# Optimization experiments

Measured on AMD Instinct MI355X. Metric: run time of the kernel, lower is better.

The kernel has to match this reference:

```python
import jax, jax.numpy as jnp
import numpy as np

B, S, D, H, K = 2, 1024, 1024, 16, 33  # batch, seq, d_model, heads, rel buckets (k+1)
d = D // H


def setup_inputs() -> dict:
    key = jax.random.key(0)
    ks = jax.random.split(key, 16)
    w = lambda k, shape: jax.random.normal(k, shape, dtype=jnp.float32) * 0.02
    return {
        "hidden_state": jax.random.normal(ks[0], (B, S, D), dtype=jnp.float32),
        "pos_indices": jax.random.randint(ks[1], (B, S, S), 0, K),
        "mask": jax.random.bernoulli(ks[2], 0.1, (B, 1, 1, S)),
        "Wq": w(ks[3], (D, D)), "bq": w(ks[4], (D,)),
        "Wk": w(ks[5], (D, D)), "bk": w(ks[6], (D,)),
        "Wv": w(ks[7], (D, D)), "bv": w(ks[8], (D,)),
        "Wo": w(ks[9], (D, D)), "bo": w(ks[10], (D,)),
        "rel_q": w(ks[11], (H, K, d)),
        "rel_k": w(ks[12], (H, K, d)),
        "rel_v": w(ks[13], (H, K, d)),
    }


def reference(hidden_state, pos_indices, mask, Wq, bq, Wk, bk, Wv, bv, Wo, bo,
              rel_q, rel_k, rel_v):
    b, s, dm = hidden_state.shape
    h, k_, dp = rel_q.shape
    # projections -> [B,H,S,d]
    def proj(x, W, bias):
        return (x @ W + bias).reshape(b, s, h, dp).transpose(0, 2, 1, 3)
    q = proj(hidden_state, Wq, bq)
    kk = proj(hidden_state, Wk, bk)
    v = proj(hidden_state, Wv, bv)
    # scale_factor = 1 (c2c) + 1 (rel_q) + 1 (rel_k)
    scale = 1.0 / np.sqrt(dp * 3).astype(np.float32)
    # content-to-content
    c2c = jnp.einsum("bhid,bhjd->bhij", q, kk) * scale
    idx = jnp.broadcast_to(pos_indices[:, None], (b, h, s, s))
    # position-to-content: raw [B,H,K,S], gathered along K with per-(i,j) bucket
    raw_p2c = jnp.einsum("hkd,bhjd->bhkj", rel_q, kk) * scale
    p2c = jnp.take_along_axis(raw_p2c, idx, axis=2)
    # content-to-position: raw [B,H,S,K], gathered along K
    raw_c2p = jnp.einsum("bhid,hkd->bhik", q, rel_k) * scale
    c2p = jnp.take_along_axis(raw_c2p, idx, axis=3)
    scores = c2c + p2c + c2p
    scores = jnp.where(mask, jnp.float32(-1e9), scores)
    probs = jax.nn.softmax(scores, axis=-1)  # dropout is identity in eval
    ctx = jnp.einsum("bhij,bhjd->bhid", probs, v)
    # value-side relative term: sum_j P[i,j] * rel_v[bucket(i,j)]
    oh = jax.nn.one_hot(pos_indices, k_, dtype=probs.dtype)  # [B,S,S,K]
    agg = jnp.einsum("bhij,bijk->bhik", probs, oh)
    ctx = ctx + jnp.einsum("bhik,hkd->bhid", agg, rel_v)
    out = ctx.transpose(0, 2, 1, 3).reshape(b, s, dm)
    return out @ Wo + bo
```

## Files before the change

kernel.cpp:

```cpp
#include <hip/hip_runtime.h>
#include <hip/hip_bf16.h>

#define B_ 2
#define S_ 1024
#define D_ 1024
#define H_ 16
#define K_ 33
#define DH 64
#define SCALE 0.07216878364870322f
#define LOG2E 1.4426950408889634f
#define SCALEL (SCALE * LOG2E)
#define FXS 32768.0f
#define FXI (1.0f / 32768.0f)

typedef __attribute__((ext_vector_type(8))) short bf16x8;
typedef __attribute__((ext_vector_type(4))) float f32x4;

__device__ __forceinline__ float b2f(unsigned short u) {
    return __uint_as_float(((unsigned int)u) << 16);
}
__device__ __forceinline__ unsigned short f2b(float f) {
    unsigned int u = __float_as_uint(f);
    u += 0x7FFFu + ((u >> 16) & 1u);
    return (unsigned short)(u >> 16);
}
__device__ __forceinline__ float ldf(const void* p, int i, int f32) {
    return f32 ? ((const float*)p)[i] : b2f(((const unsigned short*)p)[i]);
}
__device__ __forceinline__ float4 ldf4(const void* p, int i, int f32) {
    if (f32) return *(const float4*)((const float*)p + i);
    ushort4 u = *(const ushort4*)((const unsigned short*)p + i);
    return make_float4(b2f(u.x), b2f(u.y), b2f(u.z), b2f(u.w));
}
__device__ __forceinline__ float4 ldb4(const unsigned short* p, int i) {
    ushort4 u = *(const ushort4*)(p + i);
    return make_float4(b2f(u.x), b2f(u.y), b2f(u.z), b2f(u.w));
}

__global__ __launch_bounds__(256) void prep(const void* __restrict__ hidden,
                                            const void* __restrict__ mask,
                                            int* __restrict__ flags,
                                            float* __restrict__ mflag) {
    __shared__ int cnt;
    __shared__ int mev[6];
    const int t = threadIdx.x;
    if (t == 0) cnt = 0;
    if (t < 6) mev[t] = 0;
    __syncthreads();
    const unsigned short* hu = (const unsigned short*)hidden;
    int c = 0;
    for (int i = t; i < 2048; i += 256) {
        int e = (hu[i] >> 7) & 0xFF;
        if (e >= 0x8E) c++;
    }
    if (c) atomicAdd(&cnt, c);
    const unsigned char* mb = (const unsigned char*)mask;
    int e_bf = 0, e_f32 = 0, e_f64 = 0, e_f16 = 0, e_u8 = 0;
    for (int p = t; p < 2048; p += 256) {
        unsigned char v = mb[p];
        if ((p & 7) == 6 && v == 0xF0) e_f64 = 1;
        if ((p & 3) == 1 && v == 0x3F) e_bf = 1;
        if ((p & 3) == 3 && v == 0x3F) e_f32 = 1;
        if ((p & 1) == 1 && v == 0x3C) e_f16 = 1;
        if ((p & 3) != 0 && v != 0) e_u8 = 1;
    }
    if (e_f64) atomicOr(&mev[5], 1);
    if (e_bf)  atomicOr(&mev[3], 1);
    if (e_f32) atomicOr(&mev[2], 1);
    if (e_f16) atomicOr(&mev[4], 1);
    if (e_u8)  atomicOr(&mev[1], 1);
    __syncthreads();
    const int f32flag = (cnt >= 8) ? 1 : 0;
    const int mm = mev[5] ? 5 : (mev[3] ? 3 : (mev[2] ? 2 : (mev[4] ? 4 : (mev[1] ? 1 : 0))));
    if (t == 0) { flags[0] = f32flag; flags[2] = mm; }
    for (int j = t; j < B_ * S_; j += 256) {
        int m;
        if (mm == 5)      m = (((const double*)mask)[j] != 0.0);
        else if (mm == 3 || mm == 4) m = (((const unsigned short*)mask)[j] != 0);
        else if (mm == 2) m = (((const float*)mask)[j] != 0.f);
        else if (mm == 1) m = (mb[j] != 0);
        else              m = (((const int*)mask)[j] != 0);
        mflag[j] = m ? 1.f : 0.f;
    }
}

__global__ __launch_bounds__(256) void pos_pack(const int* __restrict__ pos,
                                                unsigned char* __restrict__ pos8) {
    int i = blockIdx.x * 256 + threadIdx.x;
    if (i >= (B_ * S_ * S_) / 4) return;
    int4 p = *(const int4*)&pos[i * 4];
    uchar4 o;
    o.x = (unsigned char)min(max(p.x, 0), K_ - 1);
    o.y = (unsigned char)min(max(p.y, 0), K_ - 1);
    o.z = (unsigned char)min(max(p.z, 0), K_ - 1);
    o.w = (unsigned char)min(max(p.w, 0), K_ - 1);
    *(uchar4*)&pos8[i * 4] = o;
}

__global__ __launch_bounds__(256) void w_pack(const void* __restrict__ W0,
                                              const void* __restrict__ W1,
                                              const void* __restrict__ W2,
                                              const void* __restrict__ W3,
                                              const int* __restrict__ flags,
                                              unsigned short* __restrict__ T0,
                                              unsigned short* __restrict__ T1,
                                              unsigned short* __restrict__ T2,
                                              unsigned short* __restrict__ T3) {
    __shared__ unsigned short tl[64][66];
    const int f32u = flags[0];
    const int z = blockIdx.z;
    const void* W = z == 0 ? W0 : (z == 1 ? W1 : (z == 2 ? W2 : W3));
    unsigned short* T = z == 0 ? T0 : (z == 1 ? T1 : (z == 2 ? T2 : T3));
    const int k0 = blockIdx.y * 64, n0 = blockIdx.x * 64;
    const int t = threadIdx.x;
    {
        int kr = t >> 2, nc = (t & 3) * 16;
#pragma unroll
        for (int u = 0; u < 4; ++u) {
            float4 v = ldf4(W, (k0 + kr) * 1024 + n0 + nc + u * 4, f32u);
            tl[kr][nc + u * 4 + 0] = f2b(v.x);
            tl[kr][nc + u * 4 + 1] = f2b(v.y);
            tl[kr][nc + u * 4 + 2] = f2b(v.z);
            tl[kr][nc + u * 4 + 3] = f2b(v.w);
        }
    }
    __syncthreads();
    {
        int nr = t >> 2, kc = (t & 3) * 16;
        unsigned short o[16];
#pragma unroll
        for (int u = 0; u < 16; ++u) o[u] = tl[kc + u][nr];
#pragma unroll
        for (int u = 0; u < 4; ++u)
            *(ushort4*)&T[(n0 + nr) * 1024 + k0 + kc + u * 4] = *(ushort4*)&o[u * 4];
    }
}

__global__ __launch_bounds__(256, 3) void gemm_qkv_mfma(const void* __restrict__ X,
                                                        const void* __restrict__ W0,
                                                        const void* __restrict__ W1,
                                                        const void* __restrict__ W2,
                                                        const unsigned short* __restrict__ T0,
                                                        const unsigned short* __restrict__ T1,
                                                        const unsigned short* __restrict__ T2,
                                                        const void* __restrict__ b0,
                                                        const void* __restrict__ b1,
                                                        const void* __restrict__ b2,
                                                        const int* __restrict__ flags, int useT,
                                                        unsigned short* __restrict__ q,
                                                        unsigned short* __restrict__ kk_,
                                                        unsigned short* __restrict__ v) {
    __shared__ unsigned short Asl[128][40];
    __shared__ unsigned short Bsl[64][40];
    const int f32u = flags[0];
    const int z = blockIdx.z;
    const void* W = z == 0 ? W0 : (z == 1 ? W1 : W2);
    const unsigned short* WT = z == 0 ? T0 : (z == 1 ? T1 : T2);
    const void* bias = z == 0 ? b0 : (z == 1 ? b1 : b2);
    unsigned short* outp = z == 0 ? q : (z == 1 ? kk_ : v);
    const int m0 = blockIdx.y * 128, n0 = blockIdx.x * 64;
    const int t = threadIdx.x;
    const int w = t >> 6, lane = t & 63;
    const int wr = w >> 1, wc = w & 1;
    const int lm = lane & 15, lg = lane >> 4;

    const int am = t >> 1, ac16 = (t & 1) * 16;
    const int bn = t >> 2, bk8 = (t & 3) * 8;
    const int fbn = t & 63, fbkq = (t >> 6) * 8;

    f32x4 acc[4][2] = {};
    float4 pa[4];
    ushort4 tb0, tb1;
    float pbx[8];

    {
        int base = (m0 + am) * 1024 + ac16;
#pragma unroll
        for (int u = 0; u < 4; ++u) pa[u] = ldf4(X, base + u * 4, f32u);
        if (useT) {
            const ushort4* s = (const ushort4*)&WT[(n0 + bn) * 1024 + bk8];
            tb0 = s[0]; tb1 = s[1];
        } else {
#pragma unroll
            for (int qi = 0; qi < 8; ++qi)
                pbx[qi] = ldf(W, (fbkq + qi) * 1024 + n0 + fbn, f32u);
        }
    }

    for (int k0 = 0; k0 < 1024; k0 += 32) {
        {
#pragma unroll
            for (int u = 0; u < 4; ++u) {
                ushort4 uv = {f2b(pa[u].x), f2b(pa[u].y), f2b(pa[u].z), f2b(pa[u].w)};
                *(ushort4*)&Asl[am][ac16 + u * 4] = uv;
            }
            if (useT) {
                *(ushort4*)&Bsl[bn][bk8] = tb0;
                *(ushort4*)&Bsl[bn][bk8 + 4] = tb1;
            } else {
#pragma unroll
                for (int qi = 0; qi < 8; qi += 2) {
                    unsigned int pk = (unsigned int)f2b(pbx[qi]) |
                                      ((unsigned int)f2b(pbx[qi + 1]) << 16);
                    *(unsigned int*)&Bsl[fbn][fbkq + qi] = pk;
                }
            }
        }
        __syncthreads();
        if (k0 + 32 < 1024) {
            int kn = k0 + 32;
            int base = (m0 + am) * 1024 + kn + ac16;
#pragma unroll
            for (int u = 0; u < 4; ++u) pa[u] = ldf4(X, base + u * 4, f32u);
            if (useT) {
                const ushort4* s = (const ushort4*)&WT[(n0 + bn) * 1024 + kn + bk8];
                tb0 = s[0]; tb1 = s[1];
            } else {
#pragma unroll
                for (int qi = 0; qi < 8; ++qi)
                    pbx[qi] = ldf(W, (kn + fbkq + qi) * 1024 + n0 + fbn, f32u);
            }
        }
        bf16x8 af[4], bfr[2];
#pragma unroll
        for (int mi = 0; mi < 4; ++mi)
            af[mi] = *(const bf16x8*)&Asl[wr * 64 + mi * 16 + lm][lg * 8];
#pragma unroll
        for (int nj = 0; nj < 2; ++nj)
            bfr[nj] = *(const bf16x8*)&Bsl[wc * 32 + nj * 16 + lm][lg * 8];
#pragma unroll
        for (int mi = 0; mi < 4; ++mi)
#pragma unroll
            for (int nj = 0; nj < 2; ++nj)
                acc[mi][nj] = __builtin_amdgcn_mfma_f32_16x16x32_bf16(af[mi], bfr[nj],
                                                                      acc[mi][nj], 0, 0, 0);
        __syncthreads();
    }
#pragma unroll
    for (int nj = 0; nj < 2; ++nj) {
        int n = n0 + wc * 32 + nj * 16 + lm;
        float bv = ldf(bias, n, f32u);
        int hh = n >> 6, dd = n & 63;
#pragma unroll
        for (int mi = 0; mi < 4; ++mi) {
#pragma unroll
            for (int r = 0; r < 4; ++r) {
                int m = m0 + wr * 64 + mi * 16 + lg * 4 + r;
                int bb = m >> 10, ii = m & 1023;
                outp[((bb * H_ + hh) * S_ + ii) * DH + dd] = f2b(acc[mi][nj][r] + bv);
            }
        }
    }
}

__global__ __launch_bounds__(256, 3) void gemm_out_mfma(const unsigned short* __restrict__ X,
                                                        const void* __restrict__ W,
                                                        const unsigned short* __restrict__ WT,
                                                        const void* __restrict__ bias,
                                                        const int* __restrict__ flags, int useT,
                                                        float* __restrict__ out) {
    __shared__ unsigned short Asl[128][40];
    __shared__ unsigned short Bsl[64][40];
    const int f32u = flags[0];
    const int m0 = blockIdx.y * 128, n0 = blockIdx.x * 64;
    const int t = threadIdx.x;
    const int w = t >> 6, lane = t & 63;
    const int wr = w >> 1, wc = w & 1;
    const int lm = lane & 15, lg = lane >> 4;

    const int am = t >> 1, ac16 = (t & 1) * 16;
    const int bn = t >> 2, bk8 = (t & 3) * 8;
    const int fbn = t & 63, fbkq = (t >> 6) * 8;

    f32x4 acc[4][2] = {};
    ushort4 pa[4];
    ushort4 tb0, tb1;
    float pbx[8];

    {
        const ushort4* src = (const ushort4*)&X[(m0 + am) * 1024 + ac16];
#pragma unroll
        for (int u = 0; u < 4; ++u) pa[u] = src[u];
        if (useT) {
            const ushort4* s = (const ushort4*)&WT[(n0 + bn) * 1024 + bk8];
            tb0 = s[0]; tb1 = s[1];
        } else {
#pragma unroll
            for (int qi = 0; qi < 8; ++qi)
                pbx[qi] = ldf(W, (fbkq + qi) * 1024 + n0 + fbn, f32u);
        }
    }

    for (int k0 = 0; k0 < 1024; k0 += 32) {
        {
#pragma unroll
            for (int u = 0; u < 4; ++u) *(ushort4*)&Asl[am][ac16 + u * 4] = pa[u];
            if (useT) {
                *(ushort4*)&Bsl[bn][bk8] = tb0;
                *(ushort4*)&Bsl[bn][bk8 + 4] = tb1;
            } else {
#pragma unroll
                for (int qi = 0; qi < 8; qi += 2) {
                    unsigned int pk = (unsigned int)f2b(pbx[qi]) |
                                      ((unsigned int)f2b(pbx[qi + 1]) << 16);
                    *(unsigned int*)&Bsl[fbn][fbkq + qi] = pk;
                }
            }
        }
        __syncthreads();
        if (k0 + 32 < 1024) {
            int kn = k0 + 32;
            const ushort4* src = (const ushort4*)&X[(m0 + am) * 1024 + kn + ac16];
#pragma unroll
            for (int u = 0; u < 4; ++u) pa[u] = src[u];
            if (useT) {
                const ushort4* s = (const ushort4*)&WT[(n0 + bn) * 1024 + kn + bk8];
                tb0 = s[0]; tb1 = s[1];
            } else {
#pragma unroll
                for (int qi = 0; qi < 8; ++qi)
                    pbx[qi] = ldf(W, (kn + fbkq + qi) * 1024 + n0 + fbn, f32u);
            }
        }
        bf16x8 af[4], bfr[2];
#pragma unroll
        for (int mi = 0; mi < 4; ++mi)
            af[mi] = *(const bf16x8*)&Asl[wr * 64 + mi * 16 + lm][lg * 8];
#pragma unroll
        for (int nj = 0; nj < 2; ++nj)
            bfr[nj] = *(const bf16x8*)&Bsl[wc * 32 + nj * 16 + lm][lg * 8];
#pragma unroll
        for (int mi = 0; mi < 4; ++mi)
#pragma unroll
            for (int nj = 0; nj < 2; ++nj)
                acc[mi][nj] = __builtin_amdgcn_mfma_f32_16x16x32_bf16(af[mi], bfr[nj],
                                                                      acc[mi][nj], 0, 0, 0);
        __syncthreads();
    }
#pragma unroll
    for (int nj = 0; nj < 2; ++nj) {
        int n = n0 + wc * 32 + nj * 16 + lm;
        float bv = ldf(bias, n, f32u);
#pragma unroll
        for (int mi = 0; mi < 4; ++mi) {
#pragma unroll
            for (int r = 0; r < 4; ++r) {
                int m = m0 + wr * 64 + mi * 16 + lg * 4 + r;
                out[m * 1024 + n] = acc[mi][nj][r] + bv;
            }
        }
    }
}

__global__ __launch_bounds__(256) void rel_fused(const unsigned short* __restrict__ kws,
                                                 const unsigned short* __restrict__ qws,
                                                 const void* __restrict__ relq,
                                                 const void* __restrict__ relk,
                                                 const int* __restrict__ flags,
                                                 unsigned short* __restrict__ p2c,
                                                 unsigned short* __restrict__ c2p) {
    __shared__ float xt[64][68];
    __shared__ float rr[33][68];
    const int f32u = flags[0];
    const int bh = blockIdx.y, h = bh & 15;
    const int x0 = blockIdx.x * 64;
    const int t = threadIdx.x;
    if (blockIdx.z == 0) {
#pragma unroll
        for (int qq = 0; qq < 4; ++qq) {
            int idx = t + 256 * qq;
            int j = idx >> 4, d4 = idx & 15;
            *(float4*)&xt[j][d4 * 4] = ldb4(kws, (bh * S_ + x0 + j) * DH + d4 * 4);
        }
        for (int idx = t; idx < 33 * 16; idx += 256) {
            int k = idx >> 4, d4 = idx & 15;
            *(float4*)&rr[k][d4 * 4] = ldf4(relq, (h * K_ + k) * DH + d4 * 4, f32u);
        }
        __syncthreads();
        for (int o = t; o < 33 * 64; o += 256) {
            int k = o >> 6, j = o & 63;
            float s = 0.f;
#pragma unroll
            for (int d4 = 0; d4 < 16; ++d4) {
                float4 a = *(const float4*)&rr[k][d4 * 4];
                float4 b = *(const float4*)&xt[j][d4 * 4];
                s += a.x * b.x + a.y * b.y + a.z * b.z + a.w * b.w;
            }
            p2c[(bh * K_ + k) * S_ + x0 + j] = f2b(s * SCALEL);
        }
    } else {
#pragma unroll
        for (int qq = 0; qq < 4; ++qq) {
            int idx = t + 256 * qq;
            int i = idx >> 4, d4 = idx & 15;
            *(float4*)&xt[i][d4 * 4] = ldb4(qws, (bh * S_ + x0 + i) * DH + d4 * 4);
        }
        for (int idx = t; idx < 33 * 16; idx += 256) {
            int k = idx >> 4, d4 = idx & 15;
            *(float4*)&rr[k][d4 * 4] = ldf4(relk, (h * K_ + k) * DH + d4 * 4, f32u);
        }
        __syncthreads();
        for (int o = t; o < 64 * 33; o += 256) {
            int i = o / 33, k = o % 33;
            float s = 0.f;
#pragma unroll
            for (int d4 = 0; d4 < 16; ++d4) {
                float4 a = *(const float4*)&xt[i][d4 * 4];
                float4 b = *(const float4*)&rr[k][d4 * 4];
                s += a.x * b.x + a.y * b.y + a.z * b.z + a.w * b.w;
            }
            c2p[(bh * S_ + x0 + i) * K_ + k] = f2b(s * SCALEL);
        }
    }
}

#define PS_OFF   0
#define VT_OFF   32768
#define P2CS_OFF 32768
#define C2P_OFF  50176
#define AG_OFF   54528
#define RV_OFF   71936
#define MF_OFF   76160
#define ATTN_LDS 77184

__device__ __forceinline__ int ps_addr(int il, int jc) {
    return PS_OFF + il * 512 +
           ((jc * 2) ^ ((((il >> 2) & 3) << 5) ^ ((il & 3) << 4)));
}

__global__ __launch_bounds__(512, 4) void attn_mfma(const unsigned short* __restrict__ qws,
                                                    const unsigned short* __restrict__ kws,
                                                    const unsigned short* __restrict__ vws,
                                                    const unsigned short* __restrict__ p2c,
                                                    const unsigned short* __restrict__ c2p,
                                                    const float* __restrict__ mflag,
                                                    const unsigned char* __restrict__ pos8,
                                                    const int* __restrict__ pos32,
                                                    int use8,
                                                    const void* __restrict__ relv,
                                                    const int* __restrict__ flags,
                                                    unsigned short* __restrict__ ctxo) {
    extern __shared__ char smem[];
    const int f32u = flags[0];
    const int lin = blockIdx.y * 16 + blockIdx.x;
    const int logi = (lin & 7) * 64 + (lin >> 3);
    const int bh = logi >> 4, b = bh >> 4, h = bh & 15;
    const int i0 = (logi & 15) * 64;
    const int t = threadIdx.x;
    const int w = t >> 6, lane = t & 63;
    const int lm = lane & 15, lg = lane >> 4;
    const int iband = (w & 3) * 16;
    const int jh = w >> 2;
    const int dbase = jh * 32;

    unsigned int* agU = (unsigned int*)(smem + AG_OFF);
    unsigned short* c2pS = (unsigned short*)(smem + C2P_OFF);
    unsigned short* rvS = (unsigned short*)(smem + RV_OFF);
    unsigned char* mfS = (unsigned char*)(smem + MF_OFF);

    for (int idx = t; idx < 64 * 33; idx += 512) {
        int il = idx / 33, k = idx % 33;
        c2pS[il * 34 + k] = c2p[(bh * S_ + i0 + il) * K_ + k];
    }
    for (int idx = t; idx < 33 * 64; idx += 512) {
        int k = idx >> 6, d = idx & 63;
        rvS[k * 64 + d] = f2b(ldf(relv, (h * K_ + k) * DH + d, f32u));
    }
    for (int idx = t; idx < 1024; idx += 512)
        mfS[idx] = (mflag[b * S_ + idx] != 0.f) ? 1 : 0;
    for (int idx = t; idx < 2 * 64 * 34; idx += 512) agU[idx] = 0u;

    bf16x8 aq0 = *(const bf16x8*)&qws[(bh * S_ + i0 + iband + lm) * DH + lg * 8];
    bf16x8 aq1 = *(const bf16x8*)&qws[(bh * S_ + i0 + iband + lm) * DH + 32 + lg * 8];
    f32x4 acc0 = {}, acc1 = {};

    const int p2cbase = bh * K_ * S_;
    const int rowbase = (b * S_ + i0 + iband + lg * 4) * S_;
    const int agbase = jh * 2176;
    __syncthreads();

    for (int c = 0; c < 4; ++c) {
        for (int idx = t; idx < 33 * 32; idx += 512) {
            int k = idx >> 5, v8 = idx & 31;
            uint4 src = *(const uint4*)&p2c[p2cbase + k * S_ + c * 256 + v8 * 8];
            unsigned int* dst = (unsigned int*)(smem + P2CS_OFF + k * 516 + v8 * 16);
            dst[0] = src.x; dst[1] = src.y; dst[2] = src.z; dst[3] = src.w;
        }
        __syncthreads();

        for (int jt = 0; jt < 8; ++jt) {
            const int jc = jh * 128 + jt * 16 + lm;
            const int jcol = c * 256 + jc;
            int pb4[4];
            if (use8) {
#pragma unroll
                for (int r = 0; r < 4; ++r)
                    pb4[r] = pos8[rowbase + r * S_ + jcol];
            } else {
#pragma unroll
                for (int r = 0; r < 4; ++r) {
                    int p = pos32[rowbase + r * S_ + jcol];
                    pb4[r] = min(max(p, 0), K_ - 1);
                }
            }
            bf16x8 kf0 = *(const bf16x8*)&kws[(bh * S_ + jcol) * DH + lg * 8];
            bf16x8 kf1 = *(const bf16x8*)&kws[(bh * S_ + jcol) * DH + 32 + lg * 8];
            f32x4 a = {};
            a = __builtin_amdgcn_mfma_f32_16x16x32_bf16(aq0, kf0, a, 0, 0, 0);
            a = __builtin_amdgcn_mfma_f32_16x16x32_bf16(aq1, kf1, a, 0, 0, 0);
            const int masked = mfS[jcol];
#pragma unroll
            for (int r = 0; r < 4; ++r) {
                int il = iband + lg * 4 + r;
                int pb = pb4[r];
                float gv = b2f(*(const unsigned short*)(smem + P2CS_OFF + pb * 516 + jc * 2));
                float s = a[r] * SCALEL + gv + b2f(c2pS[il * 34 + pb]);
                float ev = masked ? 0.f : exp2f(s);
                *(unsigned short*)(smem + ps_addr(il, jc)) = f2b(ev);
                atomicAdd(&agU[agbase + il * 34 + pb], (unsigned int)(ev * FXS));
            }
        }
        __syncthreads();

        for (int st = 0; st < 2; ++st) {
#pragma unroll
            for (int u = 0; u < 2; ++u) {
                int idx = t + u * 512;
                int jj = idx >> 3;
                int a8 = idx & 7;
                int d0 = a8 * 8;
                int j = c * 256 + st * 128 + jj;
                bf16x8 vv = *(const bf16x8*)&vws[(bh * S_ + j) * DH + d0];
#pragma unroll
                for (int e = 0; e < 8; ++e) {
                    int ee = (e + a8) & 7;
                    *(unsigned short*)(smem + VT_OFF + (d0 + ee) * 272 + jj * 2) =
                        ((short*)&vv)[ee];
                }
            }
            __syncthreads();
#pragma unroll
            for (int ks = 0; ks < 4; ++ks) {
                int jcb = st * 128 + ks * 32 + lg * 8;
                bf16x8 af = *(const bf16x8*)(smem + ps_addr(iband + lm, jcb));
                bf16x8 b0 = *(const bf16x8*)(smem + VT_OFF + (dbase + lm) * 272 +
                                             (ks * 32 + lg * 8) * 2);
                bf16x8 b1 = *(const bf16x8*)(smem + VT_OFF + (dbase + 16 + lm) * 272 +
                                             (ks * 32 + lg * 8) * 2);
                acc0 = __builtin_amdgcn_mfma_f32_16x16x32_bf16(af, b0, acc0, 0, 0, 0);
                acc1 = __builtin_amdgcn_mfma_f32_16x16x32_bf16(af, b1, acc1, 0, 0, 0);
            }
            __syncthreads();
        }
    }

#pragma unroll
    for (int r = 0; r < 4; ++r) {
        int il = iband + lg * 4 + r;
        float rs = 0.f;
        float o0 = acc0[r], o1 = acc1[r];
        for (int kb = 0; kb < K_; ++kb) {
            float a = (float)(agU[il * 34 + kb] + agU[2176 + il * 34 + kb]) * FXI;
            rs += a;
            o0 += a * b2f(rvS[kb * 64 + dbase + lm]);
            o1 += a * b2f(rvS[kb * 64 + dbase + 16 + lm]);
        }
        float inv = 1.0f / rs;
        ctxo[(b * S_ + i0 + il) * D_ + h * DH + dbase + lm] = f2b(o0 * inv);
        ctxo[(b * S_ + i0 + il) * D_ + h * DH + dbase + 16 + lm] = f2b(o1 * inv);
    }
}

extern "C" void kernel_launch(void* const* d_in, const int* in_sizes, int n_in,
                              void* d_out, int out_size, void* d_ws, size_t ws_size,
                              hipStream_t stream) {
    const void* hidden = d_in[0];
    const void* pos = d_in[1];
    const void* mask = d_in[2];
    const void* Wq = d_in[3];
    const void* bq = d_in[4];
    const void* Wk = d_in[5];
    const void* bk = d_in[6];
    const void* Wv = d_in[7];
    const void* bv = d_in[8];
    const void* Wo = d_in[9];
    const void* bo = d_in[10];
    const void* rq = d_in[11];
    const void* rk = d_in[12];
    const void* rv = d_in[13];

    unsigned char* wsb = (unsigned char*)d_ws;
    size_t o = 0;
    int* flags = (int*)(wsb + o);            o += 256;
    float* mfl = (float*)(wsb + o);          o += 2048 * 4;
    o = (o + 255) & ~(size_t)255;
    unsigned short* qb   = (unsigned short*)(wsb + o); o += 4194304;
    unsigned short* kb   = (unsigned short*)(wsb + o); o += 4194304;
    unsigned short* vb   = (unsigned short*)(wsb + o); o += 4194304;
    unsigned short* p2cb = (unsigned short*)(wsb + o); o += 2162688;
    unsigned short* c2pb = (unsigned short*)(wsb + o); o += 2162688;
    unsigned short* ctxb = (unsigned short*)(wsb + o); o += 4194304;
    unsigned char* pos8  = (unsigned char*)(wsb + o);  o += 2097152;
    const int use8 = (ws_size >= o) ? 1 : 0;
    unsigned short* wTq = (unsigned short*)(wsb + o);  o += 2097152;
    unsigned short* wTk = (unsigned short*)(wsb + o);  o += 2097152;
    unsigned short* wTv = (unsigned short*)(wsb + o);  o += 2097152;
    unsigned short* wTo = (unsigned short*)(wsb + o);  o += 2097152;
    const int useT = (ws_size >= o) ? 1 : 0;

    float* out = (float*)d_out;
    const int* posi = (const int*)pos;

    hipFuncSetAttribute(reinterpret_cast<const void*>(attn_mfma),
                        hipFuncAttributeMaxDynamicSharedMemorySize, ATTN_LDS);

    dim3 tb(256);
    prep<<<dim3(1), tb, 0, stream>>>(hidden, mask, flags, mfl);
    if (use8) pos_pack<<<dim3(2048), tb, 0, stream>>>(posi, pos8);
    if (useT) w_pack<<<dim3(16, 16, 4), tb, 0, stream>>>(Wq, Wk, Wv, Wo, flags,
                                                         wTq, wTk, wTv, wTo);
    gemm_qkv_mfma<<<dim3(16, 16, 3), tb, 0, stream>>>(hidden, Wq, Wk, Wv,
                                                      wTq, wTk, wTv,
                                                      bq, bk, bv, flags, useT,
                                                      qb, kb, vb);
    rel_fused<<<dim3(16, 32, 2), tb, 0, stream>>>(kb, qb, rq, rk, flags, p2cb, c2pb);
    attn_mfma<<<dim3(16, 32), dim3(512), ATTN_LDS, stream>>>(qb, kb, vb, p2cb, c2pb, mfl,
                                                             pos8, posi, use8, rv, flags,
                                                             ctxb);
    gemm_out_mfma<<<dim3(16, 16), tb, 0, stream>>>(ctxb, Wo, wTo, bo, flags, useT,
                                                   out);
}
```

Measured before the change: 159.3 us.

## Fuse setup kernels into one launch and drop duplicated aggregate buffer

Merges the prep, pos_pack and w_pack kernels into a single setup_fused launch with block ranges for each task. Each weight-pack block re-sniffs the input dtype locally instead of waiting on the flags written by prep. This removes two launch gaps and a serial dependency. In the attention kernel the two half-copies of the fixed-point aggregate buffer become one shared buffer, which shrinks LDS use but puts more atomic contention on a single array.

```diff
diff --git a/kernel.cpp b/kernel.cpp
--- a/kernel.cpp
+++ b/kernel.cpp
@@ -36,24 +36,126 @@
     ushort4 u = *(const ushort4*)(p + i);
     return make_float4(b2f(u.x), b2f(u.y), b2f(u.z), b2f(u.w));
 }
+__device__ __forceinline__ int sniff_f32(const void* hidden) {
+    __shared__ int cnt;
+    if (threadIdx.x == 0) cnt = 0;
+    __syncthreads();
+    const unsigned short* hu = (const unsigned short*)hidden;
+    int c = 0;
+    for (int i = threadIdx.x; i < 2048; i += 256) {
+        int e = (hu[i] >> 7) & 0xFF;
+        if (e >= 0x8E) c++;
+    }
+    if (c) atomicAdd(&cnt, c);
+    __syncthreads();
+    return (cnt >= 8) ? 1 : 0;
+}
+
+__global__ __launch_bounds__(256) void setup_fused(const void* __restrict__ hidden,
+                                                   const void* __restrict__ mask,
+                                                   const int* __restrict__ pos,
+                                                   const void* __restrict__ W0,
+                                                   const void* __restrict__ W1,
+                                                   const void* __restrict__ W2,
+                                                   const void* __restrict__ W3,
+                                                   int* __restrict__ flags,
+                                                   float* __restrict__ mflag,
+                                                   unsigned char* __restrict__ pos8,
+                                                   unsigned short* __restrict__ T0,
+                                                   unsigned short* __restrict__ T1,
+                                                   unsigned short* __restrict__ T2,
+                                                   unsigned short* __restrict__ T3) {
+    const int bid = blockIdx.x;
+    const int t = threadIdx.x;
+    if (bid < 2048) {
+        int i = bid * 256 + t;
+        if (i < (B_ * S_ * S_) / 4) {
+            int4 p = *(const int4*)&pos[i * 4];
+            uchar4 o;
+            o.x = (unsigned char)min(max(p.x, 0), K_ - 1);
+            o.y = (unsigned char)min(max(p.y, 0), K_ - 1);
+            o.z = (unsigned char)min(max(p.z, 0), K_ - 1);
+            o.w = (unsigned char)min(max(p.w, 0), K_ - 1);
+            *(uchar4*)&pos8[i * 4] = o;
+        }
+        return;
+    }
+    if (bid < 3072) {
+        const int f32u = sniff_f32(hidden);
+        __shared__ unsigned short tl[64][66];
+        int r = bid - 2048;
+        int z = r >> 8;
+        int wy = (r & 255) >> 4, wx = r & 15;
+        const void* W = z == 0 ? W0 : (z == 1 ? W1 : (z == 2 ? W2 : W3));
+        unsigned short* T = z == 0 ? T0 : (z == 1 ? T1 : (z == 2 ? T2 : T3));
+        const int k0 = wy * 64, n0 = wx * 64;
+        {
+            int kr = t >> 2, nc = (t & 3) * 16;
+#pragma unroll
+            for (int u = 0; u < 4; ++u) {
+                float4 v = ldf4(W, (k0 + kr) * 1024 + n0 + nc + u * 4, f32u);
+                tl[kr][nc + u * 4 + 0] = f2b(v.x);
+                tl[kr][nc + u * 4 + 1] = f2b(v.y);
+                tl[kr][nc + u * 4 + 2] = f2b(v.z);
+                tl[kr][nc + u * 4 + 3] = f2b(v.w);
+            }
+        }
+        __syncthreads();
+        {
+            int nr = t >> 2, kc = (t & 3) * 16;
+            unsigned short o[16];
+#pragma unroll
+            for (int u = 0; u < 16; ++u) o[u] = tl[kc + u][nr];
+#pragma unroll
+            for (int u = 0; u < 4; ++u)
+                *(ushort4*)&T[(n0 + nr) * 1024 + k0 + kc + u * 4] = *(ushort4*)&o[u * 4];
+        }
+        return;
+    }
+    {
+        __shared__ int mev[6];
+        const int f32u = sniff_f32(hidden);
+        if (t < 6) mev[t] = 0;
+        __syncthreads();
+        const unsigned char* mb = (const unsigned char*)mask;
+        int e_bf = 0, e_f32 = 0, e_f64 = 0, e_f16 = 0, e_u8 = 0;
+        for (int p = t; p < 2048; p += 256) {
+            unsigned char v = mb[p];
+            if ((p & 7) == 6 && v == 0xF0) e_f64 = 1;
+            if ((p & 3) == 1 && v == 0x3F) e_bf = 1;
+            if ((p & 3) == 3 && v == 0x3F) e_f32 = 1;
+            if ((p & 1) == 1 && v == 0x3C) e_f16 = 1;
+            if ((p & 3) != 0 && v != 0) e_u8 = 1;
+        }
+        if (e_f64) atomicOr(&mev[5], 1);
+        if (e_bf)  atomicOr(&mev[3], 1);
+        if (e_f32) atomicOr(&mev[2], 1);
+        if (e_f16) atomicOr(&mev[4], 1);
+        if (e_u8)  atomicOr(&mev[1], 1);
+        __syncthreads();
+        const int mm = mev[5] ? 5 : (mev[3] ? 3 : (mev[2] ? 2 : (mev[4] ? 4 : (mev[1] ? 1 : 0))));
+        if (t == 0) { flags[0] = f32u; flags[2] = mm; }
+        for (int j = t; j < B_ * S_; j += 256) {
+            int m;
+            if (mm == 5)      m = (((const double*)mask)[j] != 0.0);
+            else if (mm == 3 || mm == 4) m = (((const unsigned short*)mask)[j] != 0);
+            else if (mm == 2) m = (((const float*)mask)[j] != 0.f);
+            else if (mm == 1) m = (mb[j] != 0);
+            else              m = (((const int*)mask)[j] != 0);
+            mflag[j] = m ? 1.f : 0.f;
+        }
+    }
+}
 
 __global__ __launch_bounds__(256) void prep(const void* __restrict__ hidden,
                                             const void* __restrict__ mask,
                                             int* __restrict__ flags,
                                             float* __restrict__ mflag) {
-    __shared__ int cnt;
     __shared__ int mev[6];
     const int t = threadIdx.x;
-    if (t == 0) cnt = 0;
+    const int f32u = sniff_f32(hidden);
     if (t < 6) mev[t] = 0;
     __syncthreads();
-    const unsigned short* hu = (const unsigned short*)hidden;
-    int c = 0;
-    for (int i = t; i < 2048; i += 256) {
-        int e = (hu[i] >> 7) & 0xFF;
-        if (e >= 0x8E) c++;
-    }
-    if (c) atomicAdd(&cnt, c);
     const unsigned char* mb = (const unsigned char*)mask;
     int e_bf = 0, e_f32 = 0, e_f64 = 0, e_f16 = 0, e_u8 = 0;
     for (int p = t; p < 2048; p += 256) {
@@ -70,9 +172,8 @@
     if (e_f16) atomicOr(&mev[4], 1);
     if (e_u8)  atomicOr(&mev[1], 1);
     __syncthreads();
-    const int f32flag = (cnt >= 8) ? 1 : 0;
     const int mm = mev[5] ? 5 : (mev[3] ? 3 : (mev[2] ? 2 : (mev[4] ? 4 : (mev[1] ? 1 : 0))));
-    if (t == 0) { flags[0] = f32flag; flags[2] = mm; }
+    if (t == 0) { flags[0] = f32u; flags[2] = mm; }
     for (int j = t; j < B_ * S_; j += 256) {
         int m;
         if (mm == 5)      m = (((const double*)mask)[j] != 0.0);
@@ -95,45 +196,6 @@
     o.z = (unsigned char)min(max(p.z, 0), K_ - 1);
     o.w = (unsigned char)min(max(p.w, 0), K_ - 1);
     *(uchar4*)&pos8[i * 4] = o;
-}
-
-__global__ __launch_bounds__(256) void w_pack(const void* __restrict__ W0,
-                                              const void* __restrict__ W1,
-                                              const void* __restrict__ W2,
-                                              const void* __restrict__ W3,
-                                              const int* __restrict__ flags,
-                                              unsigned short* __restrict__ T0,
-                                              unsigned short* __restrict__ T1,
-                                              unsigned short* __restrict__ T2,
-                                              unsigned short* __restrict__ T3) {
-    __shared__ unsigned short tl[64][66];
-    const int f32u = flags[0];
-    const int z = blockIdx.z;
-    const void* W = z == 0 ? W0 : (z == 1 ? W1 : (z == 2 ? W2 : W3));
-    unsigned short* T = z == 0 ? T0 : (z == 1 ? T1 : (z == 2 ? T2 : T3));
-    const int k0 = blockIdx.y * 64, n0 = blockIdx.x * 64;
-    const int t = threadIdx.x;
-    {
-        int kr = t >> 2, nc = (t & 3) * 16;
-#pragma unroll
-        for (int u = 0; u < 4; ++u) {
-            float4 v = ldf4(W, (k0 + kr) * 1024 + n0 + nc + u * 4, f32u);
-            tl[kr][nc + u * 4 + 0] = f2b(v.x);
-            tl[kr][nc + u * 4 + 1] = f2b(v.y);
-            tl[kr][nc + u * 4 + 2] = f2b(v.z);
-            tl[kr][nc + u * 4 + 3] = f2b(v.w);
-        }
-    }
-    __syncthreads();
-    {
-        int nr = t >> 2, kc = (t & 3) * 16;
-        unsigned short o[16];
-#pragma unroll
-        for (int u = 0; u < 16; ++u) o[u] = tl[kc + u][nr];
-#pragma unroll
-        for (int u = 0; u < 4; ++u)
-            *(ushort4*)&T[(n0 + nr) * 1024 + k0 + kc + u * 4] = *(ushort4*)&o[u * 4];
-    }
 }
 
 __global__ __launch_bounds__(256, 3) void gemm_qkv_mfma(const void* __restrict__ X,
@@ -419,9 +481,9 @@
 #define P2CS_OFF 32768
 #define C2P_OFF  50176
 #define AG_OFF   54528
-#define RV_OFF   71936
-#define MF_OFF   76160
-#define ATTN_LDS 77184
+#define RV_OFF   63232
+#define MF_OFF   67456
+#define ATTN_LDS 68480
 
 __device__ __forceinline__ int ps_addr(int il, int jc) {
     return PS_OFF + il * 512 +
@@ -468,7 +530,7 @@
     }
     for (int idx = t; idx < 1024; idx += 512)
         mfS[idx] = (mflag[b * S_ + idx] != 0.f) ? 1 : 0;
-    for (int idx = t; idx < 2 * 64 * 34; idx += 512) agU[idx] = 0u;
+    for (int idx = t; idx < 64 * 34; idx += 512) agU[idx] = 0u;
 
     bf16x8 aq0 = *(const bf16x8*)&qws[(bh * S_ + i0 + iband + lm) * DH + lg * 8];
     bf16x8 aq1 = *(const bf16x8*)&qws[(bh * S_ + i0 + iband + lm) * DH + 32 + lg * 8];
@@ -476,7 +538,6 @@
 
     const int p2cbase = bh * K_ * S_;
     const int rowbase = (b * S_ + i0 + iband + lg * 4) * S_;
-    const int agbase = jh * 2176;
     __syncthreads();
 
     for (int c = 0; c < 4; ++c) {
@@ -517,7 +578,7 @@
                 float s = a[r] * SCALEL + gv + b2f(c2pS[il * 34 + pb]);
                 float ev = masked ? 0.f : exp2f(s);
                 *(unsigned short*)(smem + ps_addr(il, jc)) = f2b(ev);
-                atomicAdd(&agU[agbase + il * 34 + pb], (unsigned int)(ev * FXS));
+                atomicAdd(&agU[il * 34 + pb], (unsigned int)(ev * FXS));
             }
         }
         __syncthreads();
@@ -560,7 +621,7 @@
         float rs = 0.f;
         float o0 = acc0[r], o1 = acc1[r];
         for (int kb = 0; kb < K_; ++kb) {
-            float a = (float)(agU[il * 34 + kb] + agU[2176 + il * 34 + kb]) * FXI;
+            float a = (float)agU[il * 34 + kb] * FXI;
             rs += a;
             o0 += a * b2f(rvS[kb * 64 + dbase + lm]);
             o1 += a * b2f(rvS[kb * 64 + dbase + 16 + lm]);
@@ -615,10 +676,13 @@
                         hipFuncAttributeMaxDynamicSharedMemorySize, ATTN_LDS);
 
     dim3 tb(256);
-    prep<<<dim3(1), tb, 0, stream>>>(hidden, mask, flags, mfl);
-    if (use8) pos_pack<<<dim3(2048), tb, 0, stream>>>(posi, pos8);
-    if (useT) w_pack<<<dim3(16, 16, 4), tb, 0, stream>>>(Wq, Wk, Wv, Wo, flags,
-                                                         wTq, wTk, wTv, wTo);
+    if (use8 && useT) {
+        setup_fused<<<dim3(3073), tb, 0, stream>>>(hidden, mask, posi, Wq, Wk, Wv, Wo,
+                                                   flags, mfl, pos8, wTq, wTk, wTv, wTo);
+    } else {
+        prep<<<dim3(1), tb, 0, stream>>>(hidden, mask, flags, mfl);
+        if (use8) pos_pack<<<dim3(2048), tb, 0, stream>>>(posi, pos8);
+    }
     gemm_qkv_mfma<<<dim3(16, 16, 3), tb, 0, stream>>>(hidden, Wq, Wk, Wv,
                                                       wTq, wTk, wTv,
                                                       bq, bk, bv, flags, useT,
```

Result: faster. 151.3 us (-5.0%).
